# Kernel tuning notes

Measured on AMD Instinct MI355X. Metric: run time of the kernel, lower is better.

## Reference

```python
import jax, jax.numpy as jnp
import numpy as np

W = 256  # window size


def _stack_neighbors(x):
    """x: (b, c, w, h, d) -> (b, c, w, h, d, 3): [prev chunk, self, next chunk],
    zero-padded at sequence boundaries (matches F.pad with value=0 in Longformer)."""
    prev = jnp.pad(x[:, :-1], ((0, 0), (1, 0), (0, 0), (0, 0), (0, 0)))
    nxt = jnp.pad(x[:, 1:], ((0, 0), (0, 1), (0, 0), (0, 0), (0, 0)))
    return jnp.stack([prev, x, nxt], axis=-1)


def setup_inputs() -> dict:
    key = jax.random.key(0)
    kq, kk, kv = jax.random.split(key, 3)
    b, s, h, d = 2, 8192, 8, 64
    return {
        "query": jax.random.normal(kq, (b, s, h, d), dtype=jnp.float32),
        "key": jax.random.normal(kk, (b, s, h, d), dtype=jnp.float32),
        "value": jax.random.normal(kv, (b, s, h, d), dtype=jnp.float32),
    }


def reference(query, key, value):
    b, s, h, d = query.shape
    c = s // W
    # --- sliding_chunks_no_overlap_matmul_qk ---
    chunk_q = query.reshape(b, c, W, h, d)
    chunk_k = key.reshape(b, c, W, h, d)
    k_exp = _stack_neighbors(chunk_k)            # (b, c, W, h, d, 3)
    # (b, c, W_q, h, 3, W_k)
    diag = jnp.einsum('bcxhd,bcyhde->bcxhey', chunk_q, k_exp)
    attention = diag.reshape(b, s, h, 3 * W)
    # softmax over the 3*W window positions (dropout = identity in eval)
    attention = jax.nn.softmax(attention, axis=-1)
    # --- sliding_chunks_no_overlap_matmul_pv ---
    chunk_prob = attention.reshape(b, c, W, h, 3, W)
    chunk_v = value.reshape(b, c, W, h, d)
    v_exp = _stack_neighbors(chunk_v)            # (b, c, W, h, d, 3)
    context = jnp.einsum('bcwhpd,bcdhep->bcwhe', chunk_prob, v_exp)
    output = context.reshape(b, s, h, d)
    return output, attention
```

## Files before the change

### kernel.cpp

```cpp
#include <hip/hip_runtime.h>


#define SEQ  8192
#define NH   8
#define DM   64
#define WIN  256
#define NC   32

typedef float  f32x4  __attribute__((ext_vector_type(4)));
typedef short  bf16x8 __attribute__((ext_vector_type(8)));

__device__ __forceinline__ unsigned short bf16_rne(float x) {
    unsigned u = __builtin_bit_cast(unsigned, x);
    u += 0x7FFFu + ((u >> 16) & 1u);
    return (unsigned short)(u >> 16);
}
__device__ __forceinline__ float bf16_f32(unsigned short h) {
    unsigned u = ((unsigned)h) << 16;
    return __builtin_bit_cast(float, u);
}

__global__ __launch_bounds__(256, 2)
void wattn_mfma(const float* __restrict__ qg, const float* __restrict__ kg,
                const float* __restrict__ vg, float* __restrict__ outg,
                float* __restrict__ attng)
{
    __shared__ __align__(16) char lds[50176];

    const int t    = threadIdx.x;
    const int lane = t & 63;
    const int w    = t >> 6;
    const int a    = lane & 15;
    const int g4   = lane >> 4;

    unsigned short* vtw = (unsigned short*)(lds)         + w * 4096;
    unsigned short* plw = (unsigned short*)(lds + 32768) + w * 2048;
    float* smax = (float*)(lds + 49152);
    float* ssum = smax + 128;
    float* csc  = (float*)lds;

    int gid = blockIdx.x;
    gid = (gid & 7) * 512 + (gid >> 3);
    const int tile = gid & 7;  gid >>= 3;
    const int hh   = gid & 7;  gid >>= 3;
    const int cc   = gid & 31; gid >>= 5;
    const int bb   = gid;
    const int row0 = cc * WIN + tile * 32;

    bf16x8 qh[2][2], ql[2][2];
    #pragma unroll
    for (int rt = 0; rt < 2; ++rt)
      #pragma unroll
      for (int ks = 0; ks < 2; ++ks) {
        const float* qp = qg + (((size_t)bb * SEQ + row0 + rt*16 + a) * NH + hh) * DM
                             + ks*32 + g4*8;
        f32x4 t0 = *(const f32x4*)qp;
        f32x4 t1 = *(const f32x4*)(qp + 4);
        float f[8];
        #pragma unroll
        for (int i = 0; i < 4; ++i) { f[i] = t0[i]; f[4+i] = t1[i]; }
        #pragma unroll
        for (int i = 0; i < 8; ++i) {
            unsigned short h = bf16_rne(f[i]);
            qh[rt][ks][i] = (short)h;
            ql[rt][ks][i] = (short)bf16_rne(f[i] - bf16_f32(h));
        }
      }

    f32x4 acc[3][2][4];
    #pragma unroll
    for (int e = 0; e < 3; ++e)
      #pragma unroll
      for (int rt = 0; rt < 2; ++rt)
        #pragma unroll
        for (int ct = 0; ct < 4; ++ct)
            acc[e][rt][ct] = (f32x4){0.f, 0.f, 0.f, 0.f};

    #pragma unroll
    for (int e = 0; e < 3; ++e) {
        const int cs = cc + e - 1;
        if ((unsigned)cs < NC) {
            #pragma unroll
            for (int ct = 0; ct < 4; ++ct) {
                const float* kp = kg + (((size_t)bb * SEQ + cs*WIN + w*64 + ct*16 + a) * NH + hh) * DM;
                #pragma unroll
                for (int ks = 0; ks < 2; ++ks) {
                    f32x4 t0 = *(const f32x4*)(kp + ks*32 + g4*8);
                    f32x4 t1 = *(const f32x4*)(kp + ks*32 + g4*8 + 4);
                    float f[8];
                    #pragma unroll
                    for (int i = 0; i < 4; ++i) { f[i] = t0[i]; f[4+i] = t1[i]; }
                    bf16x8 kh, kl;
                    #pragma unroll
                    for (int i = 0; i < 8; ++i) {
                        unsigned short h = bf16_rne(f[i]);
                        kh[i] = (short)h;
                        kl[i] = (short)bf16_rne(f[i] - bf16_f32(h));
                    }
                    #pragma unroll
                    for (int rt = 0; rt < 2; ++rt) {
                        acc[e][rt][ct] = __builtin_amdgcn_mfma_f32_16x16x32_bf16(qh[rt][ks], kh, acc[e][rt][ct], 0, 0, 0);
                        acc[e][rt][ct] = __builtin_amdgcn_mfma_f32_16x16x32_bf16(qh[rt][ks], kl, acc[e][rt][ct], 0, 0, 0);
                        acc[e][rt][ct] = __builtin_amdgcn_mfma_f32_16x16x32_bf16(ql[rt][ks], kh, acc[e][rt][ct], 0, 0, 0);
                    }
                }
            }
        }
    }

    float M[2][4], INV[2][4];
    #pragma unroll
    for (int rt = 0; rt < 2; ++rt)
      #pragma unroll
      for (int reg = 0; reg < 4; ++reg) {
        float mm = -3.4e38f;
        #pragma unroll
        for (int e = 0; e < 3; ++e)
          #pragma unroll
          for (int ct = 0; ct < 4; ++ct)
            mm = fmaxf(mm, acc[e][rt][ct][reg]);
        mm = fmaxf(mm, __shfl_xor(mm, 1));
        mm = fmaxf(mm, __shfl_xor(mm, 2));
        mm = fmaxf(mm, __shfl_xor(mm, 4));
        mm = fmaxf(mm, __shfl_xor(mm, 8));
        if (a == 0) smax[(rt*16 + g4*4 + reg)*4 + w] = mm;
      }
    __syncthreads();
    #pragma unroll
    for (int rt = 0; rt < 2; ++rt)
      #pragma unroll
      for (int reg = 0; reg < 4; ++reg) {
        const float* sp = smax + (rt*16 + g4*4 + reg)*4;
        float mm = fmaxf(fmaxf(sp[0], sp[1]), fmaxf(sp[2], sp[3]));
        M[rt][reg] = mm;
        float s = 0.f;
        #pragma unroll
        for (int e = 0; e < 3; ++e)
          #pragma unroll
          for (int ct = 0; ct < 4; ++ct) {
            float p = __expf(acc[e][rt][ct][reg] - mm);
            acc[e][rt][ct][reg] = p;
            s += p;
          }
        s += __shfl_xor(s, 1);
        s += __shfl_xor(s, 2);
        s += __shfl_xor(s, 4);
        s += __shfl_xor(s, 8);
        if (a == 0) ssum[(rt*16 + g4*4 + reg)*4 + w] = s;
      }
    __syncthreads();
    #pragma unroll
    for (int rt = 0; rt < 2; ++rt)
      #pragma unroll
      for (int reg = 0; reg < 4; ++reg) {
        const float* sp = ssum + (rt*16 + g4*4 + reg)*4;
        INV[rt][reg] = 1.0f / (sp[0] + sp[1] + sp[2] + sp[3]);
      }

    #pragma unroll
    for (int rt = 0; rt < 2; ++rt)
      #pragma unroll
      for (int reg = 0; reg < 4; ++reg) {
        const float iv = INV[rt][reg];
        float* ab = attng + (((size_t)bb * SEQ + row0 + rt*16 + g4*4 + reg) * NH + hh) * 768
                          + w*64 + a;
        #pragma unroll
        for (int e = 0; e < 3; ++e)
          #pragma unroll
          for (int ct = 0; ct < 4; ++ct) {
            float p = acc[e][rt][ct][reg] * iv;
            acc[e][rt][ct][reg] = p;
            __builtin_nontemporal_store(p, ab + e*256 + ct*16);
          }
      }

    f32x4 acc2[2][4];
    #pragma unroll
    for (int rt = 0; rt < 2; ++rt)
      #pragma unroll
      for (int dt = 0; dt < 4; ++dt)
        acc2[rt][dt] = (f32x4){0.f, 0.f, 0.f, 0.f};

    #pragma unroll
    for (int e = 0; e < 3; ++e) {
        const int cs = cc + e - 1;
        if ((unsigned)cs < NC) {
            __syncthreads();
            #pragma unroll
            for (int i = 0; i < 16; ++i) {
                const int kk = i*4 + g4;
                const float* vp = vg + (((size_t)bb * SEQ + cs*WIN + w*64 + kk) * NH + hh) * DM
                                     + a*4;
                f32x4 v4 = *(const f32x4*)vp;
                #pragma unroll
                for (int j = 0; j < 4; ++j) {
                    const int d = a*4 + j;
                    vtw[(d>>4)*1024 + (kk>>3)*128 + (d&15)*8 + (kk&7)] = bf16_rne(v4[j]);
                }
            }
            #pragma unroll
            for (int rt = 0; rt < 2; ++rt)
              #pragma unroll
              for (int reg = 0; reg < 4; ++reg) {
                const int prow = rt*16 + g4*4 + reg;
                #pragma unroll
                for (int ct = 0; ct < 4; ++ct) {
                    const int key = ct*16 + a;
                    plw[prow*64 + (((key>>3) ^ (prow&7)) << 3) + (key&7)] =
                        bf16_rne(acc[e][rt][ct][reg]);
                }
              }
            __syncthreads();
            #pragma unroll
            for (int ks = 0; ks < 2; ++ks) {
                bf16x8 pa[2], vb[4];
                #pragma unroll
                for (int rt = 0; rt < 2; ++rt) {
                    const int prow = rt*16 + a;
                    pa[rt] = *(const bf16x8*)(plw + prow*64 + ((((ks<<2) + g4) ^ (prow&7)) << 3));
                }
                #pragma unroll
                for (int dt = 0; dt < 4; ++dt)
                    vb[dt] = *(const bf16x8*)(vtw + dt*1024 + ((ks<<2) + g4)*128 + a*8);
                #pragma unroll
                for (int rt = 0; rt < 2; ++rt)
                  #pragma unroll
                  for (int dt = 0; dt < 4; ++dt)
                    acc2[rt][dt] = __builtin_amdgcn_mfma_f32_16x16x32_bf16(pa[rt], vb[dt], acc2[rt][dt], 0, 0, 0);
            }
        }
    }

    __syncthreads();
    #pragma unroll
    for (int rt = 0; rt < 2; ++rt)
      #pragma unroll
      for (int dt = 0; dt < 4; ++dt)
        #pragma unroll
        for (int reg = 0; reg < 4; ++reg)
          csc[w*2176 + (rt*16 + g4*4 + reg)*68 + dt*16 + a] = acc2[rt][dt][reg];
    __syncthreads();
    #pragma unroll
    for (int r = 0; r < 8; ++r) {
        const int row = w*8 + r;
        float s = csc[          row*68 + lane] + csc[  2176 + row*68 + lane]
                + csc[2*2176 + row*68 + lane] + csc[3*2176 + row*68 + lane];
        __builtin_nontemporal_store(
            s, outg + (((size_t)bb * SEQ + row0 + row) * NH + hh) * DM + lane);
    }
}

extern "C" void kernel_launch(void* const* d_in, const int* in_sizes, int n_in,
                              void* d_out, int out_size, void* d_ws, size_t ws_size,
                              hipStream_t stream) {
    const float* q = (const float*)d_in[0];
    const float* k = (const float*)d_in[1];
    const float* v = (const float*)d_in[2];

    float* out  = (float*)d_out;
    float* attn = (float*)d_out + (size_t)2 * SEQ * NH * DM;

    dim3 grid(2 * NC * NH * (WIN / 32));
    dim3 block(256);
    wattn_mfma<<<grid, block, 0, stream>>>(q, k, v, out, attn);
}
```

Before: 669.9 us.

## Precompute bf16 hi/lo K split and transposed bf16 V in a prep kernel

Adds a prep kernel that converts K into bf16 high and low halves and writes V transposed in bf16 into the workspace. The main kernel then loads these directly from global memory instead of converting and staging them through LDS in every block, which shrinks LDS use and removes conversion work that was repeated across the many tiles sharing the same K/V chunks. In exchange it costs an extra launch and an extra pass over global memory for the prepared buffers. The old kernel is kept as a fallback when the workspace is too small.

After: 638.8 us. 4.6% less time.

```diff
diff --git a/kernel.cpp b/kernel.cpp
--- a/kernel.cpp
+++ b/kernel.cpp
@@ -9,15 +9,258 @@
 
 typedef float  f32x4  __attribute__((ext_vector_type(4)));
 typedef short  bf16x8 __attribute__((ext_vector_type(8)));
-
-__device__ __forceinline__ unsigned short bf16_rne(float x) {
+typedef short  bf16x4 __attribute__((ext_vector_type(4)));
+typedef unsigned short u16;
+
+__device__ __forceinline__ u16 bf16_rne(float x) {
     unsigned u = __builtin_bit_cast(unsigned, x);
     u += 0x7FFFu + ((u >> 16) & 1u);
-    return (unsigned short)(u >> 16);
+    return (u16)(u >> 16);
 }
-__device__ __forceinline__ float bf16_f32(unsigned short h) {
+__device__ __forceinline__ float bf16_f32(u16 h) {
     unsigned u = ((unsigned)h) << 16;
     return __builtin_bit_cast(float, u);
+}
+
+__global__ __launch_bounds__(256)
+void wattn_prep(const float* __restrict__ kg, const float* __restrict__ vg,
+                u16* __restrict__ khp, u16* __restrict__ klp, u16* __restrict__ vtp)
+{
+    __shared__ float tile[64 * 68];
+    const int bid = blockIdx.x;
+    const int t   = threadIdx.x;
+
+    if (bid < 4096) {
+        const size_t base = (size_t)bid * 2048 + t * 8;
+        f32x4 a0 = *(const f32x4*)(kg + base);
+        f32x4 a1 = *(const f32x4*)(kg + base + 4);
+        bf16x8 h, l;
+        #pragma unroll
+        for (int i = 0; i < 8; ++i) {
+            float f = (i < 4) ? a0[i] : a1[i - 4];
+            u16 hh = bf16_rne(f);
+            h[i] = (short)hh;
+            l[i] = (short)bf16_rne(f - bf16_f32(hh));
+        }
+        *(bf16x8*)(khp + base) = h;
+        *(bf16x8*)(klp + base) = l;
+    } else {
+        const int vid = bid - 4096;
+        const int st  = vid & 127;
+        const int hh  = (vid >> 7) & 7;
+        const int bb  = vid >> 10;
+        const int s0  = st * 64;
+
+        const int r  = t >> 2;
+        const int dg = (t & 3) * 16;
+        const float* vp = vg + (((size_t)bb * SEQ + s0 + r) * NH + hh) * DM + dg;
+        #pragma unroll
+        for (int i = 0; i < 4; ++i)
+            *(f32x4*)&tile[r * 68 + dg + 4 * i] = *(const f32x4*)(vp + 4 * i);
+        __syncthreads();
+
+        const int d  = t >> 2;
+        const int sg = (t & 3) * 16;
+        u16* op = vtp + (((size_t)bb * NH + hh) * DM + d) * SEQ + s0 + sg;
+        bf16x8 o0, o1;
+        #pragma unroll
+        for (int j = 0; j < 8; ++j) o0[j] = (short)bf16_rne(tile[(sg + j) * 68 + d]);
+        #pragma unroll
+        for (int j = 0; j < 8; ++j) o1[j] = (short)bf16_rne(tile[(sg + 8 + j) * 68 + d]);
+        *(bf16x8*)op       = o0;
+        *(bf16x8*)(op + 8) = o1;
+    }
+}
+
+__global__ __launch_bounds__(256, 2)
+void wattn_mfma2(const float* __restrict__ qg, const u16* __restrict__ khp,
+                 const u16* __restrict__ klp, const u16* __restrict__ vtp,
+                 float* __restrict__ outg, float* __restrict__ attng)
+{
+    __shared__ __align__(16) char lds[35840];
+
+    const int t    = threadIdx.x;
+    const int lane = t & 63;
+    const int w    = t >> 6;
+    const int a    = lane & 15;
+    const int g4   = lane >> 4;
+
+    u16*   pw   = (u16*)(lds) + w * 2304;
+    float* csc  = (float*)lds;
+    float* smax = (float*)(lds + 34816);
+    float* ssum = smax + 128;
+
+    int gid = blockIdx.x;
+    gid = (gid & 7) * 512 + (gid >> 3);
+    const int tile = gid & 7;  gid >>= 3;
+    const int hh   = gid & 7;  gid >>= 3;
+    const int cc   = gid & 31; gid >>= 5;
+    const int bb   = gid;
+    const int row0 = cc * WIN + tile * 32;
+
+    bf16x8 qh[2][2], ql[2][2];
+    #pragma unroll
+    for (int rt = 0; rt < 2; ++rt)
+      #pragma unroll
+      for (int ks = 0; ks < 2; ++ks) {
+        const float* qp = qg + (((size_t)bb * SEQ + row0 + rt*16 + a) * NH + hh) * DM
+                             + ks*32 + g4*8;
+        f32x4 t0 = *(const f32x4*)qp;
+        f32x4 t1 = *(const f32x4*)(qp + 4);
+        #pragma unroll
+        for (int i = 0; i < 8; ++i) {
+            float f = (i < 4) ? t0[i] : t1[i - 4];
+            u16 hv = bf16_rne(f);
+            qh[rt][ks][i] = (short)hv;
+            ql[rt][ks][i] = (short)bf16_rne(f - bf16_f32(hv));
+        }
+      }
+
+    f32x4 acc[3][4][2];
+    #pragma unroll
+    for (int e = 0; e < 3; ++e)
+      #pragma unroll
+      for (int ct = 0; ct < 4; ++ct)
+        #pragma unroll
+        for (int rt = 0; rt < 2; ++rt)
+            acc[e][ct][rt] = (f32x4){0.f, 0.f, 0.f, 0.f};
+
+    #pragma unroll
+    for (int e = 0; e < 3; ++e) {
+        const int cs = cc + e - 1;
+        if ((unsigned)cs < NC) {
+            #pragma unroll
+            for (int ct = 0; ct < 4; ++ct) {
+                const size_t koff = (((size_t)bb * SEQ + cs*WIN + w*64 + ct*16 + a) * NH + hh) * DM
+                                  + g4*8;
+                #pragma unroll
+                for (int ks = 0; ks < 2; ++ks) {
+                    bf16x8 kh = *(const bf16x8*)(khp + koff + ks*32);
+                    bf16x8 kl = *(const bf16x8*)(klp + koff + ks*32);
+                    #pragma unroll
+                    for (int rt = 0; rt < 2; ++rt) {
+                        acc[e][ct][rt] = __builtin_amdgcn_mfma_f32_16x16x32_bf16(kh, qh[rt][ks], acc[e][ct][rt], 0, 0, 0);
+                        acc[e][ct][rt] = __builtin_amdgcn_mfma_f32_16x16x32_bf16(kh, ql[rt][ks], acc[e][ct][rt], 0, 0, 0);
+                        acc[e][ct][rt] = __builtin_amdgcn_mfma_f32_16x16x32_bf16(kl, qh[rt][ks], acc[e][ct][rt], 0, 0, 0);
+                    }
+                }
+            }
+        }
+    }
+
+    float M[2], INV[2];
+    #pragma unroll
+    for (int rt = 0; rt < 2; ++rt) {
+        float mm = 0.f;
+        #pragma unroll
+        for (int e = 0; e < 3; ++e)
+          #pragma unroll
+          for (int ct = 0; ct < 4; ++ct)
+            #pragma unroll
+            for (int reg = 0; reg < 4; ++reg)
+              mm = fmaxf(mm, acc[e][ct][rt][reg]);
+        mm = fmaxf(mm, __shfl_xor(mm, 16));
+        mm = fmaxf(mm, __shfl_xor(mm, 32));
+        if (g4 == 0) smax[(rt*16 + a)*4 + w] = mm;
+    }
+    __syncthreads();
+    #pragma unroll
+    for (int rt = 0; rt < 2; ++rt) {
+        const float* sp = smax + (rt*16 + a)*4;
+        float mm = fmaxf(fmaxf(sp[0], sp[1]), fmaxf(sp[2], sp[3]));
+        M[rt] = mm;
+        float s = 0.f;
+        #pragma unroll
+        for (int e = 0; e < 3; ++e)
+          #pragma unroll
+          for (int ct = 0; ct < 4; ++ct)
+            #pragma unroll
+            for (int reg = 0; reg < 4; ++reg) {
+                float p = __expf(acc[e][ct][rt][reg] - mm);
+                acc[e][ct][rt][reg] = p;
+                s += p;
+            }
+        s += __shfl_xor(s, 16);
+        s += __shfl_xor(s, 32);
+        if (g4 == 0) ssum[(rt*16 + a)*4 + w] = s;
+    }
+    __syncthreads();
+    #pragma unroll
+    for (int rt = 0; rt < 2; ++rt) {
+        const float* sp = ssum + (rt*16 + a)*4;
+        INV[rt] = 1.0f / (sp[0] + sp[1] + sp[2] + sp[3]);
+    }
+
+    #pragma unroll
+    for (int rt = 0; rt < 2; ++rt) {
+        float* ab = attng + (((size_t)bb * SEQ + row0 + rt*16 + a) * NH + hh) * 768
+                          + w*64 + g4*4;
+        #pragma unroll
+        for (int e = 0; e < 3; ++e)
+          #pragma unroll
+          for (int ct = 0; ct < 4; ++ct) {
+            f32x4 p = acc[e][ct][rt] * INV[rt];
+            acc[e][ct][rt] = p;
+            __builtin_nontemporal_store(p, (f32x4*)(ab + e*256 + ct*16));
+          }
+    }
+
+    f32x4 acc2[4][2];
+    #pragma unroll
+    for (int dt = 0; dt < 4; ++dt)
+      #pragma unroll
+      for (int rt = 0; rt < 2; ++rt)
+        acc2[dt][rt] = (f32x4){0.f, 0.f, 0.f, 0.f};
+
+    #pragma unroll
+    for (int e = 0; e < 3; ++e) {
+        const int cs = cc + e - 1;
+        if ((unsigned)cs < NC) {
+            #pragma unroll
+            for (int rt = 0; rt < 2; ++rt)
+              #pragma unroll
+              for (int ct = 0; ct < 4; ++ct) {
+                f32x4 p = acc[e][ct][rt];
+                bf16x4 pk;
+                #pragma unroll
+                for (int reg = 0; reg < 4; ++reg) pk[reg] = (short)bf16_rne(p[reg]);
+                *(bf16x4*)(pw + (rt*16 + a)*72 + ct*16 + g4*4) = pk;
+              }
+            #pragma unroll
+            for (int ks = 0; ks < 2; ++ks) {
+                bf16x8 pb[2], va[4];
+                #pragma unroll
+                for (int rt = 0; rt < 2; ++rt)
+                    pb[rt] = *(const bf16x8*)(pw + (rt*16 + a)*72 + ks*32 + g4*8);
+                #pragma unroll
+                for (int dt = 0; dt < 4; ++dt)
+                    va[dt] = *(const bf16x8*)(vtp
+                        + (((size_t)bb * NH + hh) * DM + dt*16 + a) * SEQ
+                        + cs*WIN + w*64 + ks*32 + g4*8);
+                #pragma unroll
+                for (int dt = 0; dt < 4; ++dt)
+                  #pragma unroll
+                  for (int rt = 0; rt < 2; ++rt)
+                    acc2[dt][rt] = __builtin_amdgcn_mfma_f32_16x16x32_bf16(va[dt], pb[rt], acc2[dt][rt], 0, 0, 0);
+            }
+        }
+    }
+
+    __syncthreads();
+    #pragma unroll
+    for (int dt = 0; dt < 4; ++dt)
+      #pragma unroll
+      for (int rt = 0; rt < 2; ++rt)
+        *(f32x4*)&csc[w*2176 + (rt*16 + a)*68 + dt*16 + g4*4] = acc2[dt][rt];
+    __syncthreads();
+    #pragma unroll
+    for (int r = 0; r < 8; ++r) {
+        const int row = w*8 + r;
+        float s = csc[          row*68 + lane] + csc[  2176 + row*68 + lane]
+                + csc[2*2176 + row*68 + lane] + csc[3*2176 + row*68 + lane];
+        __builtin_nontemporal_store(
+            s, outg + (((size_t)bb * SEQ + row0 + row) * NH + hh) * DM + lane);
+    }
 }
 
 __global__ __launch_bounds__(256, 2)
@@ -26,7 +269,6 @@
                 float* __restrict__ attng)
 {
     __shared__ __align__(16) char lds[50176];
-
     const int t    = threadIdx.x;
     const int lane = t & 63;
     const int w    = t >> 6;
@@ -260,7 +502,16 @@
     float* out  = (float*)d_out;
     float* attn = (float*)d_out + (size_t)2 * SEQ * NH * DM;
 
-    dim3 grid(2 * NC * NH * (WIN / 32));
-    dim3 block(256);
-    wattn_mfma<<<grid, block, 0, stream>>>(q, k, v, out, attn);
+    const size_t NELEM = (size_t)2 * SEQ * NH * DM;
+    const size_t NEED  = 3 * NELEM * sizeof(u16);
+
+    if (ws_size >= NEED) {
+        u16* khp = (u16*)d_ws;
+        u16* klp = khp + NELEM;
+        u16* vtp = klp + NELEM;
+        wattn_prep<<<dim3(6144), dim3(256), 0, stream>>>(k, v, khp, klp, vtp);
+        wattn_mfma2<<<dim3(4096), dim3(256), 0, stream>>>(q, khp, klp, vtp, out, attn);
+    } else {
+        wattn_mfma<<<dim3(4096), dim3(256), 0, stream>>>(q, k, v, out, attn);
+    }
 }
```
